# Kernel optimization log

Measured on AMD Instinct MI355X. Metric: run time of the kernel, lower is better.

Reference implementation:

```python
import jax, jax.numpy as jnp
import numpy as np

D = 256      # input channels
DK = 64      # key/query/value channels
BS, W, H = 8, 64, 64


def setup_inputs() -> dict:
    key = jax.random.key(0)
    k1, k2, k3, k4 = jax.random.split(key, 4)
    v = jax.random.normal(k1, (BS, D, W, H), dtype=jnp.float32)
    # conv1x1 weights collapse to plain matrices over the channel dim
    Wqkv = jax.random.normal(k2, (3 * DK, D), dtype=jnp.float32) * 0.02
    Wout = jax.random.normal(k3, (D, DK), dtype=jnp.float32) * 0.02
    gamma = jax.random.normal(k4, (1,), dtype=jnp.float32)  # original inits to 0; nonzero for a non-degenerate baseline
    return {"v": v, "Wqkv": Wqkv, "Wout": Wout, "gamma": gamma}


def reference(v, Wqkv, Wout, gamma):
    bs, c, w, h = v.shape
    n = w * h
    d_k = Wout.shape[1]
    x = v.reshape(bs, c, n)                      # (b, c, n)
    qkv = jnp.einsum('oc,bcn->bon', Wqkv, x)      # 1x1 conv == channel matmul
    q = qkv[:, :d_k]                              # (b, dk, n)
    k = qkv[:, d_k:2 * d_k]
    val = qkv[:, 2 * d_k:]
    s = jnp.einsum('bdi,bdj->bij', q, k)          # (b, n, n) = query^T key
    beta = jax.nn.softmax(s, axis=2)              # exp(s - logsumexp(s, axis=2))
    y = jnp.einsum('bdi,bij->bdj', val, beta)     # bmm(value, beta)
    o = jnp.einsum('od,bdn->bon', Wout, y) * gamma[0] + x
    return o.reshape(bs, c, w, h)
```

## Files before the change

### kernel.cpp

```cpp
#include <hip/hip_runtime.h>

typedef unsigned short ushort_t;
typedef __bf16 bf16x8 __attribute__((ext_vector_type(8)));
typedef short short4v __attribute__((ext_vector_type(4)));
typedef float f32x4 __attribute__((ext_vector_type(4)));
typedef unsigned int uint4v __attribute__((ext_vector_type(4)));
typedef unsigned int uint2v __attribute__((ext_vector_type(2)));

#define NTOK 4096
#define DMODEL 256
#define DK 64
#define BS 8
#define LN2INV 1.44269504088896f

__device__ __forceinline__ ushort_t f2bf(float f) {
  unsigned u = __builtin_bit_cast(unsigned, f);
  u += 0x7fffu + ((u >> 16) & 1u);
  return (ushort_t)(u >> 16);
}
__device__ __forceinline__ float bf2f(ushort_t s) {
  return __builtin_bit_cast(float, ((unsigned)s) << 16);
}
__device__ __forceinline__ bf16x8 lds_frag(const ushort_t* p) {
  return __builtin_bit_cast(bf16x8, *(const uint4v*)p);
}
__device__ __forceinline__ bf16x8 ldg8(const ushort_t* p) {
  return __builtin_bit_cast(bf16x8, *(const uint4v*)p);
}
__device__ __forceinline__ short4v lo8(uint4v v) {
  uint2v t; t.x = v.x; t.y = v.y;
  return __builtin_bit_cast(short4v, t);
}
__device__ __forceinline__ short4v hi8(uint4v v) {
  uint2v t; t.x = v.z; t.y = v.w;
  return __builtin_bit_cast(short4v, t);
}
__device__ __forceinline__ float fexp2(float x) {
#if __has_builtin(__builtin_amdgcn_exp2f)
  return __builtin_amdgcn_exp2f(x);
#else
  return exp2f(x);
#endif
}
__device__ __forceinline__ unsigned bfpack(float x, float y) {
  return __builtin_amdgcn_perm(__builtin_bit_cast(unsigned, y),
                               __builtin_bit_cast(unsigned, x), 0x07060302u);
}
__device__ __forceinline__ f32x4 mfma16(short4v a, short4v b, f32x4 c) {
#if defined(__HIP_DEVICE_COMPILE__)
#if __has_builtin(__builtin_amdgcn_mfma_f32_16x16x16bf16_1k)
  return __builtin_amdgcn_mfma_f32_16x16x16bf16_1k(a, b, c, 0, 0, 0);
#else
  typedef __bf16 bf16x4 __attribute__((ext_vector_type(4)));
  return __builtin_amdgcn_mfma_f32_16x16x16_bf16(__builtin_bit_cast(bf16x4, a),
                                                 __builtin_bit_cast(bf16x4, b), c, 0, 0, 0);
#endif
#else
  (void)a; (void)b;
  return c;
#endif
}

typedef __attribute__((address_space(3))) unsigned int lds_u32;
typedef const __attribute__((address_space(1))) unsigned int glob_u32;
__device__ __forceinline__ void gll16(const void* g, void* l) {
#if defined(__HIP_DEVICE_COMPILE__)
  __builtin_amdgcn_global_load_lds((glob_u32*)g, (lds_u32*)l, 16, 0, 0);
#else
  (void)g; (void)l;
#endif
}

__global__ __launch_bounds__(256) void k_convert(const float* __restrict__ Wqkv,
                                                 const float* __restrict__ Wout,
                                                 ushort_t* __restrict__ Wb,
                                                 ushort_t* __restrict__ Woutb) {
  int i = blockIdx.x * 256 + threadIdx.x;
  if (i < 3 * DK * DMODEL) {
    float w = Wqkv[i];
    if (i < DK * DMODEL) w *= LN2INV;
    Wb[i] = f2bf(w);
  } else {
    int j = i - 3 * DK * DMODEL;
    Woutb[j] = f2bf(Wout[j]);
  }
}

__global__ __launch_bounds__(256) void k_qkv(const float* __restrict__ x,
                                             const ushort_t* __restrict__ W,
                                             ushort_t* __restrict__ QT,
                                             ushort_t* __restrict__ KT,
                                             ushort_t* __restrict__ Vf) {
  const int b = blockIdx.y;
  const int n0 = blockIdx.x * 64;
  const int tid = threadIdx.x;
  const int lane = tid & 63, wv = tid >> 6;
  const int quad = lane >> 4, l15 = lane & 15;
  __shared__ __align__(16) ushort_t lx[64 * 264];
  __shared__ __align__(16) ushort_t t[64 * 72];

  const float* xb = x + (size_t)b * DMODEL * NTOK;

#pragma unroll 1
  for (int cc = 0; cc < 4; cc++) {
    const int c0chunk = cc * 64;
#pragma unroll
    for (int kr = 0; kr < 2; kr++) {
      int s = tid + 256 * kr;
      int c = s >> 3, ns = (s & 7) * 8;
      const float* src = xb + (size_t)(c0chunk + c) * NTOK + n0 + ns;
      f32x4 a = *(const f32x4*)src;
      f32x4 bq = *(const f32x4*)(src + 4);
      uint4v o;
      o.x = (unsigned)f2bf(a[0]) | ((unsigned)f2bf(a[1]) << 16);
      o.y = (unsigned)f2bf(a[2]) | ((unsigned)f2bf(a[3]) << 16);
      o.z = (unsigned)f2bf(bq[0]) | ((unsigned)f2bf(bq[1]) << 16);
      o.w = (unsigned)f2bf(bq[2]) | ((unsigned)f2bf(bq[3]) << 16);
      *(uint4v*)(t + c * 72 + ns) = o;
    }
    __syncthreads();
#pragma unroll
    for (int kr = 0; kr < 2; kr++) {
      int s = tid + 256 * kr;
      int n = s >> 3, cs = (s & 7) * 8;
      unsigned e0 = t[(cs + 0) * 72 + n], e1 = t[(cs + 1) * 72 + n];
      unsigned e2 = t[(cs + 2) * 72 + n], e3 = t[(cs + 3) * 72 + n];
      unsigned e4 = t[(cs + 4) * 72 + n], e5 = t[(cs + 5) * 72 + n];
      unsigned e6 = t[(cs + 6) * 72 + n], e7 = t[(cs + 7) * 72 + n];
      uint4v o;
      o.x = e0 | (e1 << 16); o.y = e2 | (e3 << 16);
      o.z = e4 | (e5 << 16); o.w = e6 | (e7 << 16);
      *(uint4v*)(lx + n * 264 + c0chunk + cs) = o;
    }
    __syncthreads();
  }

  f32x4 acc[3][4];
  const f32x4 zero4 = {0.f, 0.f, 0.f, 0.f};
#pragma unroll
  for (int i = 0; i < 3; i++)
#pragma unroll
    for (int j = 0; j < 4; j++) acc[i][j] = zero4;

#pragma unroll
  for (int c0 = 0; c0 < DMODEL; c0 += 32) {
    bf16x8 aw[3];
#pragma unroll
    for (int mt = 0; mt < 3; mt++)
      aw[mt] = ldg8(W + (wv * 48 + mt * 16 + l15) * DMODEL + c0 + quad * 8);
    bf16x8 bb[4];
#pragma unroll
    for (int nt = 0; nt < 4; nt++)
      bb[nt] = lds_frag(lx + (nt * 16 + l15) * 264 + c0 + quad * 8);
#pragma unroll
    for (int mt = 0; mt < 3; mt++)
#pragma unroll
      for (int nt = 0; nt < 4; nt++)
        acc[mt][nt] = __builtin_amdgcn_mfma_f32_16x16x32_bf16(aw[mt], bb[nt], acc[mt][nt], 0, 0, 0);
  }

  __syncthreads();
  ushort_t* qk_t = lx;
  ushort_t* v_t = lx + 128 * 68;
#pragma unroll
  for (int mt = 0; mt < 3; mt++) {
    int o = wv * 48 + mt * 16 + quad * 4;
#pragma unroll
    for (int nt = 0; nt < 4; nt++) {
      int nl = nt * 16 + l15;
      f32x4 v4 = acc[mt][nt];
      if (o < 128) {
        uint2v ww;
        ww.x = (unsigned)f2bf(v4[0]) | ((unsigned)f2bf(v4[1]) << 16);
        ww.y = (unsigned)f2bf(v4[2]) | ((unsigned)f2bf(v4[3]) << 16);
        int row = (o < 64) ? nl : 64 + nl;
        *(uint2v*)(qk_t + row * 68 + (o & 63)) = ww;
      } else {
        int dbase = o - 128;
        int idx = (nt * 2 + (dbase >> 5)) * 512 + ((l15 >> 2) << 7) +
                  ((dbase & 15) << 3) + (((dbase >> 4) & 1) << 2) + (l15 & 3);
#pragma unroll
        for (int r = 0; r < 4; r++) v_t[idx + (r << 3)] = f2bf(v4[r]);
      }
    }
  }
  __syncthreads();
  {
    ushort_t* QTb = QT + ((size_t)b * NTOK + n0) * DK;
    ushort_t* KTb = KT + ((size_t)b * NTOK + n0) * DK;
#pragma unroll
    for (int k = 0; k < 4; k++) {
      int s = tid + 256 * k;
      int row = s >> 3, seg = (s & 7) * 8;
      uint4v val = *(const uint4v*)(qk_t + row * 68 + seg);
      ushort_t* dst = (row < 64) ? (QTb + (size_t)row * DK + seg)
                                 : (KTb + (size_t)(row - 64) * DK + seg);
      *(uint4v*)dst = val;
    }
    ushort_t* Vtile = Vf + ((size_t)b * 64 + (n0 >> 6)) * 4096;
    *(uint4v*)(Vtile + tid * 8) = *(const uint4v*)(v_t + tid * 8);
    *(uint4v*)(Vtile + 2048 + tid * 8) = *(const uint4v*)(v_t + 2048 + tid * 8);
  }
}

__global__ __launch_bounds__(512, 4) void k_rsum(const ushort_t* __restrict__ QT,
                                                 const ushort_t* __restrict__ KT,
                                                 float* __restrict__ Rr) {
  const int id = blockIdx.x;
  const int b = id & 7;
  const int i0 = (id >> 3) * 64;
  const int tid = threadIdx.x;
  const int lane = tid & 63, wv = tid >> 6;
  const int quad = lane >> 4, l15 = lane & 15;
  __shared__ __align__(16) float partial[8 * 64];
  const ushort_t* QTb = QT + ((size_t)b * NTOK + i0) * DK;
  const ushort_t* KTb = KT + ((size_t)b * NTOK + wv * 512) * DK;

  bf16x8 aq0[4], aq1[4];
#pragma unroll
  for (int isub = 0; isub < 4; isub++) {
    const ushort_t* qp = QTb + (size_t)(isub * 16 + l15) * DK + quad * 8;
    aq0[isub] = ldg8(qp);
    aq1[isub] = ldg8(qp + 32);
  }

  f32x4 racc[4];
  const f32x4 zero4 = {0.f, 0.f, 0.f, 0.f};
#pragma unroll
  for (int isub = 0; isub < 4; isub++) racc[isub] = zero4;

#pragma unroll 1
  for (int ph = 0; ph < 8; ph++) {
    const ushort_t* kb_base = KTb + (size_t)ph * 64 * DK;
    bf16x8 kb0[4], kb1[4];
#pragma unroll
    for (int nt = 0; nt < 4; nt++) {
      const ushort_t* kp = kb_base + (size_t)(nt * 16 + l15) * DK + quad * 8;
      kb0[nt] = ldg8(kp);
      kb1[nt] = ldg8(kp + 32);
    }
#pragma unroll
    for (int isub = 0; isub < 4; isub++)
#pragma unroll
      for (int nt = 0; nt < 4; nt++) {
        f32x4 s4 = __builtin_amdgcn_mfma_f32_16x16x32_bf16(aq0[isub], kb0[nt], zero4, 0, 0, 0);
        s4 = __builtin_amdgcn_mfma_f32_16x16x32_bf16(aq1[isub], kb1[nt], s4, 0, 0, 0);
        racc[isub][0] += fexp2(s4[0]);
        racc[isub][1] += fexp2(s4[1]);
        racc[isub][2] += fexp2(s4[2]);
        racc[isub][3] += fexp2(s4[3]);
      }
  }

#pragma unroll
  for (int isub = 0; isub < 4; isub++)
#pragma unroll
    for (int r = 0; r < 4; r++) {
      float v = racc[isub][r];
      v += __shfl_xor(v, 1);
      v += __shfl_xor(v, 2);
      v += __shfl_xor(v, 4);
      v += __shfl_xor(v, 8);
      racc[isub][r] = v;
    }
  if (l15 == 0) {
#pragma unroll
    for (int isub = 0; isub < 4; isub++)
      *(f32x4*)(partial + wv * 64 + isub * 16 + quad * 4) = racc[isub];
  }
  __syncthreads();
  if (tid < 64) {
    float s = 0.f;
#pragma unroll
    for (int w = 0; w < 8; w++) s += partial[w * 64 + tid];
    Rr[(size_t)b * NTOK + i0 + tid] = -__log2f(s);
  }
}

__global__ __launch_bounds__(512, 4) void k_pv(const ushort_t* __restrict__ QT,
                                               const ushort_t* __restrict__ KT,
                                               const ushort_t* __restrict__ Vf,
                                               const float* __restrict__ Rr,
                                               const ushort_t* __restrict__ Wout,
                                               const float* __restrict__ gammap,
                                               const float* __restrict__ x,
                                               float* __restrict__ outp) {
  const int id = blockIdx.x;
  const int b = id & 7;
  const int j0 = (id >> 3) * 64;
  const int tid = threadIdx.x;
  const int lane = tid & 63, wv = tid >> 6;
  const int quad = lane >> 4, l15 = lane & 15;
  const int ih = wv >> 2, wq = wv & 3;

  __shared__ __align__(16) ushort_t pool[24576];
  float* lrtab = (float*)pool;
  ushort_t* wbuf = pool + 8192 + wv * 2048;
  float* rbufA = (float*)pool;
  float* rbufB = (float*)(pool + 8704);
  ushort_t* pbuf = pool + 17408;

  const ushort_t* KTb = KT + ((size_t)b * NTOK + j0) * DK;
  const ushort_t* QTb = QT + ((size_t)b * NTOK + ih * 2048) * DK;
  const ushort_t* Vfb = Vf + ((size_t)b * 64 + ih * 32) * 4096;
  const float* Rrb = Rr + (size_t)b * NTOK;

  const int qrow = (wq * 16 + l15) * DK + quad * 8;
  const int vfo = wq * 1024 + lane * 8;

  gll16(QTb + qrow,       wbuf);
  gll16(QTb + qrow + 32,  wbuf + 512);
  gll16(Vfb + vfo,        wbuf + 1024);
  gll16(Vfb + vfo + 512,  wbuf + 1536);

  {
    f32x4 r0 = *(const f32x4*)(Rrb + tid * 8);
    f32x4 r1 = *(const f32x4*)(Rrb + tid * 8 + 4);
    *(f32x4*)(lrtab + tid * 8) = r0;
    *(f32x4*)(lrtab + tid * 8 + 4) = r1;
  }

  bf16x8 kb0[4], kb1[4];
#pragma unroll
  for (int nt = 0; nt < 4; nt++) {
    const ushort_t* kp = KTb + (size_t)(nt * 16 + l15) * DK + quad * 8;
    kb0[nt] = ldg8(kp);
    kb1[nt] = ldg8(kp + 32);
  }

  __syncthreads();

  f32x4 yt[4][4];
  const f32x4 zero4 = {0.f, 0.f, 0.f, 0.f};
#pragma unroll
  for (int i = 0; i < 4; i++)
#pragma unroll
    for (int j = 0; j < 4; j++) yt[i][j] = zero4;

#pragma unroll 1
  for (int it = 0; it < 32; it++) {
    const int cb = it & 1, nb = cb ^ 1;
    const int tpre = (it + 1 < 32) ? it + 1 : 31;
    {
      const ushort_t* qp = QTb + (size_t)tpre * 64 * DK + qrow;
      const ushort_t* vp = Vfb + (size_t)tpre * 4096 + vfo;
      ushort_t* nbuf = wbuf + nb * 2048;
      gll16(qp,       nbuf);
      gll16(qp + 32,  nbuf + 512);
      gll16(vp,       nbuf + 1024);
      gll16(vp + 512, nbuf + 1536);
    }
    asm volatile("s_waitcnt vmcnt(4)" ::: "memory");
    __builtin_amdgcn_sched_barrier(0);
    const ushort_t* cbuf = wbuf + cb * 2048;
    bf16x8 a0 = lds_frag(cbuf + lane * 8);
    bf16x8 a1 = lds_frag(cbuf + 512 + lane * 8);
    uint4v vv0 = *(const uint4v*)(cbuf + 1024 + lane * 8);
    uint4v vv1 = *(const uint4v*)(cbuf + 1536 + lane * 8);
    f32x4 lrv = *(const f32x4*)(lrtab + ih * 2048 + it * 64 + wq * 16 + quad * 4);
    short4v vf0 = lo8(vv0), vf1 = hi8(vv0), vf2 = lo8(vv1), vf3 = hi8(vv1);
#pragma unroll
    for (int nt = 0; nt < 4; nt++) {
      f32x4 s4 = __builtin_amdgcn_mfma_f32_16x16x32_bf16(a0, kb0[nt], lrv, 0, 0, 0);
      s4 = __builtin_amdgcn_mfma_f32_16x16x32_bf16(a1, kb1[nt], s4, 0, 0, 0);
      uint2v wp;
      wp.x = bfpack(fexp2(s4[0]), fexp2(s4[1]));
      wp.y = bfpack(fexp2(s4[2]), fexp2(s4[3]));
      short4v wf = __builtin_bit_cast(short4v, wp);
      yt[nt][0] = mfma16(wf, vf0, yt[nt][0]);
      yt[nt][1] = mfma16(wf, vf1, yt[nt][1]);
      yt[nt][2] = mfma16(wf, vf2, yt[nt][2]);
      yt[nt][3] = mfma16(wf, vf3, yt[nt][3]);
    }
  }

  asm volatile("s_waitcnt vmcnt(0)" ::: "memory");
  __syncthreads();

  float* rb = (ih == 0) ? rbufA : rbufB;
  if (wq == 0) {
#pragma unroll
    for (int nt = 0; nt < 4; nt++)
#pragma unroll
      for (int dsub = 0; dsub < 4; dsub++)
        *(f32x4*)(rb + (dsub * 16 + l15) * 68 + nt * 16 + quad * 4) = yt[nt][dsub];
  }
  __syncthreads();
  if (wq == 1) {
#pragma unroll
    for (int nt = 0; nt < 4; nt++)
#pragma unroll
      for (int dsub = 0; dsub < 4; dsub++) {
        float* p = rb + (dsub * 16 + l15) * 68 + nt * 16 + quad * 4;
        *(f32x4*)p = *(const f32x4*)p + yt[nt][dsub];
      }
  }
  __syncthreads();
  if (wq == 2) {
#pragma unroll
    for (int nt = 0; nt < 4; nt++)
#pragma unroll
      for (int dsub = 0; dsub < 4; dsub++) {
        float* p = rb + (dsub * 16 + l15) * 68 + nt * 16 + quad * 4;
        *(f32x4*)p = *(const f32x4*)p + yt[nt][dsub];
      }
  }
  __syncthreads();
  if (wq == 3) {
#pragma unroll
    for (int nt = 0; nt < 4; nt++)
#pragma unroll
      for (int dsub = 0; dsub < 4; dsub++) {
        float* p = rb + (dsub * 16 + l15) * 68 + nt * 16 + quad * 4;
        *(f32x4*)p = *(const f32x4*)p + yt[nt][dsub];
      }
  }
  __syncthreads();
  {
    const int nt = wv & 3;
#pragma unroll
    for (int k = 0; k < 2; k++) {
      const int dsub = (wv >> 2) * 2 + k;
      const float* pA = rbufA + (dsub * 16 + l15) * 68 + nt * 16 + quad * 4;
      const float* pB = rbufB + (dsub * 16 + l15) * 68 + nt * 16 + quad * 4;
      f32x4 v4 = *(const f32x4*)pA + *(const f32x4*)pB;
#pragma unroll
      for (int r = 0; r < 4; r++)
        pbuf[(nt * 16 + quad * 4 + r) * 72 + dsub * 16 + l15] = f2bf(v4[r]);
    }
  }
  __syncthreads();

  bf16x8 yb0[4], yb1[4];
#pragma unroll
  for (int nt = 0; nt < 4; nt++) {
    yb0[nt] = lds_frag(pbuf + (nt * 16 + l15) * 72 + quad * 8);
    yb1[nt] = lds_frag(pbuf + (nt * 16 + l15) * 72 + 32 + quad * 8);
  }
  f32x4 oacc[2][4];
#pragma unroll
  for (int m = 0; m < 2; m++)
#pragma unroll
    for (int nt = 0; nt < 4; nt++) oacc[m][nt] = zero4;
#pragma unroll
  for (int m = 0; m < 2; m++) {
    int c = (wv * 2 + m) * 16 + l15;
    bf16x8 aw0 = __builtin_bit_cast(bf16x8, *(const uint4v*)(Wout + c * DK + quad * 8));
    bf16x8 aw1 = __builtin_bit_cast(bf16x8, *(const uint4v*)(Wout + c * DK + 32 + quad * 8));
#pragma unroll
    for (int nt = 0; nt < 4; nt++) {
      oacc[m][nt] = __builtin_amdgcn_mfma_f32_16x16x32_bf16(aw0, yb0[nt], oacc[m][nt], 0, 0, 0);
      oacc[m][nt] = __builtin_amdgcn_mfma_f32_16x16x32_bf16(aw1, yb1[nt], oacc[m][nt], 0, 0, 0);
    }
  }
  float g = gammap[0];
  const float* xb = x + (size_t)b * DMODEL * NTOK;
  float* ob = outp + (size_t)b * DMODEL * NTOK;
#pragma unroll
  for (int m = 0; m < 2; m++) {
    int cbase = (wv * 2 + m) * 16 + quad * 4;
#pragma unroll
    for (int nt = 0; nt < 4; nt++) {
      int n = j0 + nt * 16 + l15;
#pragma unroll
      for (int r = 0; r < 4; r++) {
        size_t idx = (size_t)(cbase + r) * NTOK + n;
        ob[idx] = oacc[m][nt][r] * g + xb[idx];
      }
    }
  }
}

extern "C" void kernel_launch(void* const* d_in, const int* in_sizes, int n_in,
                              void* d_out, int out_size, void* d_ws, size_t ws_size,
                              hipStream_t stream) {
  const float* v = (const float*)d_in[0];
  const float* Wqkv = (const float*)d_in[1];
  const float* Wout = (const float*)d_in[2];
  const float* gamma = (const float*)d_in[3];
  float* outp = (float*)d_out;

  ushort_t* QT = (ushort_t*)d_ws;
  ushort_t* KT = QT + (size_t)BS * NTOK * DK;
  ushort_t* Vf = KT + (size_t)BS * NTOK * DK;
  ushort_t* Wb = Vf + (size_t)BS * DK * NTOK;
  ushort_t* Woutb = Wb + 3 * DK * DMODEL;
  float* Rr = (float*)(Woutb + DMODEL * DK);

  k_convert<<<dim3(256), 256, 0, stream>>>(Wqkv, Wout, Wb, Woutb);
  k_qkv<<<dim3(64, BS), 256, 0, stream>>>(v, Wb, QT, KT, Vf);
  k_rsum<<<dim3(512), 512, 0, stream>>>(QT, KT, Rr);
  k_pv<<<dim3(512), 512, 0, stream>>>(QT, KT, Vf, Rr, Woutb, gamma, v, outp);
}
```

Before: 185.3 us.

## Split row-sum kernel over key halves with LDS double-buffered key prefetch

The softmax row-sum kernel is split into twice as many 256-thread blocks, each covering half the keys, and writes partial sums. The log of the combined sum now happens when the PV kernel loads its table. Inside the loop, key tiles are fetched asynchronously into double-buffered LDS so global loads overlap the MFMA and exp work, replacing direct register loads. This is meant to hide load latency and raise the number of resident waves, at the cost of an extra partial buffer and a few more loads in k_pv.

Result: no change. 188.1 us (+1.5%).

```diff
diff --git a/kernel.cpp b/kernel.cpp
--- a/kernel.cpp
+++ b/kernel.cpp
@@ -203,18 +203,31 @@
   }
 }
 
-__global__ __launch_bounds__(512, 4) void k_rsum(const ushort_t* __restrict__ QT,
+__global__ __launch_bounds__(256, 4) void k_rsum(const ushort_t* __restrict__ QT,
                                                  const ushort_t* __restrict__ KT,
-                                                 float* __restrict__ Rr) {
+                                                 float* __restrict__ Rp) {
   const int id = blockIdx.x;
   const int b = id & 7;
-  const int i0 = (id >> 3) * 64;
+  const int i0 = ((id >> 3) & 63) * 64;
+  const int jh = id >> 9;
   const int tid = threadIdx.x;
   const int lane = tid & 63, wv = tid >> 6;
   const int quad = lane >> 4, l15 = lane & 15;
-  __shared__ __align__(16) float partial[8 * 64];
+
+  __shared__ __align__(16) ushort_t pool[16384];
+  ushort_t* wbuf = pool + wv * 4096;
+  float* partial = (float*)pool;
+
   const ushort_t* QTb = QT + ((size_t)b * NTOK + i0) * DK;
-  const ushort_t* KTb = KT + ((size_t)b * NTOK + wv * 512) * DK;
+  const ushort_t* KTb = KT + ((size_t)b * NTOK + jh * 2048 + wv * 512) * DK;
+
+  {
+    const ushort_t* kp = KTb + (size_t)l15 * DK + quad * 8;
+    gll16(kp,            wbuf);
+    gll16(kp + 32,       wbuf + 512);
+    gll16(kp + 16 * DK,  wbuf + 1024);
+    gll16(kp + 16 * DK + 32, wbuf + 1536);
+  }
 
   bf16x8 aq0[4], aq1[4];
 #pragma unroll
@@ -224,33 +237,51 @@
     aq1[isub] = ldg8(qp + 32);
   }
 
+  __syncthreads();
+
   f32x4 racc[4];
   const f32x4 zero4 = {0.f, 0.f, 0.f, 0.f};
 #pragma unroll
   for (int isub = 0; isub < 4; isub++) racc[isub] = zero4;
 
 #pragma unroll 1
-  for (int ph = 0; ph < 8; ph++) {
-    const ushort_t* kb_base = KTb + (size_t)ph * 64 * DK;
-    bf16x8 kb0[4], kb1[4];
-#pragma unroll
-    for (int nt = 0; nt < 4; nt++) {
-      const ushort_t* kp = kb_base + (size_t)(nt * 16 + l15) * DK + quad * 8;
-      kb0[nt] = ldg8(kp);
-      kb1[nt] = ldg8(kp + 32);
-    }
-#pragma unroll
-    for (int isub = 0; isub < 4; isub++)
-#pragma unroll
-      for (int nt = 0; nt < 4; nt++) {
-        f32x4 s4 = __builtin_amdgcn_mfma_f32_16x16x32_bf16(aq0[isub], kb0[nt], zero4, 0, 0, 0);
-        s4 = __builtin_amdgcn_mfma_f32_16x16x32_bf16(aq1[isub], kb1[nt], s4, 0, 0, 0);
-        racc[isub][0] += fexp2(s4[0]);
-        racc[isub][1] += fexp2(s4[1]);
-        racc[isub][2] += fexp2(s4[2]);
-        racc[isub][3] += fexp2(s4[3]);
-      }
-  }
+  for (int ph = 0; ph < 16; ph++) {
+    const int cb = ph & 1, nb = cb ^ 1;
+    const int ppre = (ph + 1 < 16) ? ph + 1 : 15;
+    {
+      const ushort_t* kp = KTb + (size_t)(ppre * 32 + l15) * DK + quad * 8;
+      ushort_t* nbuf = wbuf + nb * 2048;
+      gll16(kp,                nbuf);
+      gll16(kp + 32,           nbuf + 512);
+      gll16(kp + 16 * DK,      nbuf + 1024);
+      gll16(kp + 16 * DK + 32, nbuf + 1536);
+    }
+    asm volatile("s_waitcnt vmcnt(4)" ::: "memory");
+    __builtin_amdgcn_sched_barrier(0);
+    const ushort_t* cbuf = wbuf + cb * 2048;
+    bf16x8 kb00 = lds_frag(cbuf + lane * 8);
+    bf16x8 kb01 = lds_frag(cbuf + 512 + lane * 8);
+    bf16x8 kb10 = lds_frag(cbuf + 1024 + lane * 8);
+    bf16x8 kb11 = lds_frag(cbuf + 1536 + lane * 8);
+#pragma unroll
+    for (int isub = 0; isub < 4; isub++) {
+      f32x4 s4 = __builtin_amdgcn_mfma_f32_16x16x32_bf16(aq0[isub], kb00, zero4, 0, 0, 0);
+      s4 = __builtin_amdgcn_mfma_f32_16x16x32_bf16(aq1[isub], kb01, s4, 0, 0, 0);
+      racc[isub][0] += fexp2(s4[0]);
+      racc[isub][1] += fexp2(s4[1]);
+      racc[isub][2] += fexp2(s4[2]);
+      racc[isub][3] += fexp2(s4[3]);
+      f32x4 t4 = __builtin_amdgcn_mfma_f32_16x16x32_bf16(aq0[isub], kb10, zero4, 0, 0, 0);
+      t4 = __builtin_amdgcn_mfma_f32_16x16x32_bf16(aq1[isub], kb11, t4, 0, 0, 0);
+      racc[isub][0] += fexp2(t4[0]);
+      racc[isub][1] += fexp2(t4[1]);
+      racc[isub][2] += fexp2(t4[2]);
+      racc[isub][3] += fexp2(t4[3]);
+    }
+  }
+
+  asm volatile("s_waitcnt vmcnt(0)" ::: "memory");
+  __syncthreads();
 
 #pragma unroll
   for (int isub = 0; isub < 4; isub++)
@@ -270,17 +301,15 @@
   }
   __syncthreads();
   if (tid < 64) {
-    float s = 0.f;
-#pragma unroll
-    for (int w = 0; w < 8; w++) s += partial[w * 64 + tid];
-    Rr[(size_t)b * NTOK + i0 + tid] = -__log2f(s);
+    float s = partial[tid] + partial[64 + tid] + partial[128 + tid] + partial[192 + tid];
+    Rp[((size_t)jh * BS + b) * NTOK + i0 + tid] = s;
   }
 }
 
 __global__ __launch_bounds__(512, 4) void k_pv(const ushort_t* __restrict__ QT,
                                                const ushort_t* __restrict__ KT,
                                                const ushort_t* __restrict__ Vf,
-                                               const float* __restrict__ Rr,
+                                               const float* __restrict__ Rp,
                                                const ushort_t* __restrict__ Wout,
                                                const float* __restrict__ gammap,
                                                const float* __restrict__ x,
@@ -303,7 +332,6 @@
   const ushort_t* KTb = KT + ((size_t)b * NTOK + j0) * DK;
   const ushort_t* QTb = QT + ((size_t)b * NTOK + ih * 2048) * DK;
   const ushort_t* Vfb = Vf + ((size_t)b * 64 + ih * 32) * 4096;
-  const float* Rrb = Rr + (size_t)b * NTOK;
 
   const int qrow = (wq * 16 + l15) * DK + quad * 8;
   const int vfo = wq * 1024 + lane * 8;
@@ -314,10 +342,20 @@
   gll16(Vfb + vfo + 512,  wbuf + 1536);
 
   {
-    f32x4 r0 = *(const f32x4*)(Rrb + tid * 8);
-    f32x4 r1 = *(const f32x4*)(Rrb + tid * 8 + 4);
-    *(f32x4*)(lrtab + tid * 8) = r0;
-    *(f32x4*)(lrtab + tid * 8 + 4) = r1;
+    const float* Rp0 = Rp + (size_t)b * NTOK;
+    const float* Rp1 = Rp + (size_t)BS * NTOK + (size_t)b * NTOK;
+    f32x4 a0 = *(const f32x4*)(Rp0 + tid * 8);
+    f32x4 a1 = *(const f32x4*)(Rp0 + tid * 8 + 4);
+    f32x4 b0 = *(const f32x4*)(Rp1 + tid * 8);
+    f32x4 b1 = *(const f32x4*)(Rp1 + tid * 8 + 4);
+    f32x4 s0, s1;
+#pragma unroll
+    for (int r = 0; r < 4; r++) {
+      s0[r] = -__log2f(a0[r] + b0[r]);
+      s1[r] = -__log2f(a1[r] + b1[r]);
+    }
+    *(f32x4*)(lrtab + tid * 8) = s0;
+    *(f32x4*)(lrtab + tid * 8 + 4) = s1;
   }
 
   bf16x8 kb0[4], kb1[4];
@@ -485,10 +523,10 @@
   ushort_t* Vf = KT + (size_t)BS * NTOK * DK;
   ushort_t* Wb = Vf + (size_t)BS * DK * NTOK;
   ushort_t* Woutb = Wb + 3 * DK * DMODEL;
-  float* Rr = (float*)(Woutb + DMODEL * DK);
+  float* Rp = (float*)(Woutb + DMODEL * DK);
 
   k_convert<<<dim3(256), 256, 0, stream>>>(Wqkv, Wout, Wb, Woutb);
   k_qkv<<<dim3(64, BS), 256, 0, stream>>>(v, Wb, QT, KT, Vf);
-  k_rsum<<<dim3(512), 512, 0, stream>>>(QT, KT, Rr);
-  k_pv<<<dim3(512), 512, 0, stream>>>(QT, KT, Vf, Rr, Woutb, gamma, v, outp);
-}
+  k_rsum<<<dim3(1024), 256, 0, stream>>>(QT, KT, Rp);
+  k_pv<<<dim3(512), 512, 0, stream>>>(QT, KT, Vf, Rp, Woutb, gamma, v, outp);
+}
```
